# Kernel optimization log

Measured on AMD Instinct MI355X. Metric: run time of the kernel, lower is better.

The kernel has to match this reference:

```python
import jax, jax.numpy as jnp
import numpy as np

L, D, DB, P, B = 33, 2048, 1024, 24, 2048
EPS = 1e-5

def _ln(x, g, b):
    # LayerNorm over last axis, eps matches torch default 1e-5
    mu = jnp.mean(x, axis=-1, keepdims=True)
    var = jnp.mean(jnp.square(x - mu), axis=-1, keepdims=True)
    return (x - mu) * jax.lax.rsqrt(var + EPS) * g + b

def setup_inputs() -> dict:
    key = jax.random.key(0)
    ks = jax.random.split(key, 8)
    s1 = 1.0 / np.sqrt(D)   # fan-in style scaling to keep activations sane
    s2 = 1.0 / np.sqrt(DB)
    sp = 1.0 / np.sqrt(P)
    return {
        "x":      jax.random.normal(ks[0], (B, L, D), jnp.float32),
        "pos_emb": jax.random.uniform(ks[1], (L, P), jnp.float32),
        "Wk":     jax.random.normal(ks[2], (P, D), jnp.float32) * sp,
        "W1":     jax.random.normal(ks[3], (L, D, DB), jnp.float32) * s1,
        "b1":     jnp.zeros((L, DB), jnp.float32),
        "ln1_g":  jnp.ones((L, DB), jnp.float32),
        "ln1_b":  jnp.zeros((L, DB), jnp.float32),
        "W2":     jax.random.normal(ks[4], (L, DB, D), jnp.float32) * s2,
        "b2":     jnp.zeros((L, D), jnp.float32),
        "ln2_g":  jnp.ones((L, D), jnp.float32),
        "ln2_b":  jnp.zeros((L, D), jnp.float32),
        "Wq1":    jax.random.normal(ks[5], (D, DB), jnp.float32) * s1,
        "bq1":    jnp.zeros((DB,), jnp.float32),
        "lnq_g":  jnp.ones((DB,), jnp.float32),
        "lnq_b":  jnp.zeros((DB,), jnp.float32),
        "Wq2":    jax.random.normal(ks[6], (DB, D), jnp.float32) * s2,
        "bq2":    jnp.zeros((D,), jnp.float32),
    }

def reference(x, pos_emb, Wk, W1, b1, ln1_g, ln1_b, W2, b2, ln2_g, ln2_b,
              Wq1, bq1, lnq_g, lnq_b, Wq2, bq2):
    # x: [B, L, D]
    z_L = x[:, -1, :]                                   # [B, D]
    keys = pos_emb @ Wk                                 # Eq.10: [L, D]
    # Eq.11 + Eq.4: per-layer value MLPs, grouped as batched GEMMs
    h = jax.nn.gelu(jnp.einsum('bld,ldk->blk', x, W1) + b1, approximate=False)
    h = _ln(h, ln1_g, ln1_b)                            # [B, L, DB]
    v = jnp.einsum('blk,lkd->bld', h, W2) + b2          # [B, L, D]
    values = _ln(v, ln2_g, ln2_b)                       # [B, L, D]
    # Eq.5: query from last layer
    hq = jax.nn.gelu(z_L @ Wq1 + bq1, approximate=False)
    hq = _ln(hq, lnq_g, lnq_b)
    q_tr = hq @ Wq2 + bq2                               # [B, D]
    query = 1.0 + jax.nn.elu(z_L + q_tr)                # [B, D]
    # Eq.7-9: single-query attention over depth + residual
    attn = jax.nn.softmax(query @ keys.T, axis=-1)      # [B, L]
    attended = jnp.einsum('bl,bld->bd', attn, values)   # [B, D]
    return z_L + attended
```

## Files before the change

kernel.cpp:

```cpp
#include <hip/hip_runtime.h>
#include <cstddef>
#include <cstdint>

#define Lc 33
#define Dc 2048
#define DBc 1024
#define Pc 24
#define Bc 2048

typedef __attribute__((ext_vector_type(4))) float f32x4;
typedef __attribute__((ext_vector_type(8))) short s16x8;
typedef __attribute__((ext_vector_type(4))) short s16x4;

__device__ __forceinline__ short bf16r(float f) {
  unsigned u = __float_as_uint(f);
  u = (u + 0x7fffu + ((u >> 16) & 1u)) >> 16;
  return (short)u;
}
__device__ __forceinline__ float bf2f(short s) {
  return __uint_as_float(((unsigned)(unsigned short)s) << 16);
}
__device__ __forceinline__ s16x8 pack8(const float* f) {
  s16x8 r;
#pragma unroll
  for (int i = 0; i < 8; ++i) r[i] = bf16r(f[i]);
  return r;
}
__device__ __forceinline__ void split8(const float* f, s16x8& hi, s16x8& lo) {
#pragma unroll
  for (int i = 0; i < 8; ++i) {
    short h = bf16r(f[i]);
    hi[i] = h;
    lo[i] = bf16r(f[i] - bf2f(h));
  }
}
__device__ __forceinline__ void gl_lds16(const void* g, void* l) {
  __builtin_amdgcn_global_load_lds(
      (const __attribute__((address_space(1))) unsigned int*)g,
      (__attribute__((address_space(3))) unsigned int*)l, 16, 0, 0);
}

__global__ __launch_bounds__(256)
void cvt_bf16_kernel(const float* __restrict__ in,
                     unsigned short* __restrict__ outp) {
  const size_t i = ((size_t)blockIdx.x * 256 + threadIdx.x) * 8;
  f32x4 a = *(const f32x4*)(in + i);
  f32x4 b = *(const f32x4*)(in + i + 4);
  float f[8] = {a[0], a[1], a[2], a[3], b[0], b[1], b[2], b[3]};
  *(s16x8*)(outp + i) = pack8(f);
}

__global__ __launch_bounds__(256)
void keys_kernel(const float* __restrict__ pe, const float* __restrict__ Wk,
                 float* __restrict__ keys) {
  const int l = blockIdx.x;
  const int d = blockIdx.y * 256 + threadIdx.x;
  float s = 0.f;
#pragma unroll
  for (int p = 0; p < Pc; ++p) s += pe[l * Pc + p] * Wk[(size_t)p * Dc + d];
  keys[(size_t)l * Dc + d] = s;
}

template <int K, int N>
__global__ __launch_bounds__(256)
void transpose_w(const float* __restrict__ W, unsigned short* __restrict__ Wt) {
  const int z = blockIdx.z;
  const int k0 = blockIdx.x * 64, n0 = blockIdx.y * 64;
  __shared__ unsigned short tile[64][66];
  const int t = threadIdx.x;
  {
    const int r = t >> 2, cq = (t & 3) * 16;
    const float* src = W + (size_t)z * K * N + (size_t)(k0 + r) * N + n0 + cq;
#pragma unroll
    for (int i = 0; i < 16; i += 4) {
      f32x4 v = *(const f32x4*)(src + i);
#pragma unroll
      for (int j = 0; j < 4; ++j)
        tile[r][cq + i + j] = (unsigned short)bf16r(v[j]);
    }
  }
  __syncthreads();
  {
    const int n = t >> 2, kc = (t & 3) * 16;
    s16x8 o0, o1;
#pragma unroll
    for (int i = 0; i < 8; ++i) {
      o0[i] = tile[kc + i][n];
      o1[i] = tile[kc + 8 + i][n];
    }
    unsigned short* dst =
        Wt + (size_t)z * N * K + (size_t)(n0 + n) * K + k0 + kc;
    *(s16x8*)dst = o0;
    *(s16x8*)(dst + 8) = o1;
  }
}

template <int K, int N, int GELU>
__global__ __launch_bounds__(256, 2)
void gemm2ph(const unsigned short* __restrict__ A,
             const unsigned short* __restrict__ Wt,
             const float* __restrict__ bias,
             unsigned short* __restrict__ outbuf) {
  constexpr int NT = K / 64;
  const int z = blockIdx.z, bm = blockIdx.x, bn = blockIdx.y;
  const int tid = threadIdx.x, lane = tid & 63, w = tid >> 6;
  const int wr = (w >> 1) * 64, wc = (w & 1) * 64;
  const int l15 = lane & 15, kb = lane >> 4;

  __shared__ __align__(16) unsigned short Als[2][128 * 64];
  __shared__ __align__(16) unsigned short Bls[2][128 * 64];

  f32x4 acc[4][4];
#pragma unroll
  for (int m = 0; m < 4; ++m)
#pragma unroll
    for (int n = 0; n < 4; ++n) {
      acc[m][n][0] = 0.f; acc[m][n][1] = 0.f;
      acc[m][n][2] = 0.f; acc[m][n][3] = 0.f;
    }

  const int rl8 = lane >> 3, sl = lane & 7;
  const int swzE = ((sl ^ rl8) << 3);

  const unsigned short* Bbase = Wt + (size_t)z * N * K;

  auto stage = [&](int buf, int kt) {
#pragma unroll
    for (int j = 0; j < 4; ++j) {
      const int rloc = w * 32 + j * 8 + rl8;
      gl_lds16(A + ((size_t)(bm * 128 + rloc) * Lc + z) * K + kt * 64 + swzE,
               (char*)&Als[buf][0] + w * 4096 + j * 1024);
      gl_lds16(Bbase + (size_t)(bn * 128 + rloc) * K + kt * 64 + swzE,
               (char*)&Bls[buf][0] + w * 4096 + j * 1024);
    }
  };

  stage(0, 0);
  asm volatile("s_waitcnt vmcnt(0)" ::: "memory");
  __builtin_amdgcn_s_barrier();

  for (int kt = 0; kt < NT; ++kt) {
    const int cur = kt & 1;
    if (kt + 1 < NT) stage(cur ^ 1, kt + 1);
#pragma unroll
    for (int kk = 0; kk < 2; ++kk) {
      s16x8 af[4], bfv[4];
#pragma unroll
      for (int m = 0; m < 4; ++m) {
        const int row = wr + m * 16 + l15;
        const int slot = kk * 4 + kb;
        af[m] = *(const s16x8*)((const char*)&Als[cur][0] + row * 128 +
                                ((slot ^ (row & 7)) << 4));
      }
#pragma unroll
      for (int n = 0; n < 4; ++n) {
        const int row = wc + n * 16 + l15;
        const int slot = kk * 4 + kb;
        bfv[n] = *(const s16x8*)((const char*)&Bls[cur][0] + row * 128 +
                                 ((slot ^ (row & 7)) << 4));
      }
#pragma unroll
      for (int m = 0; m < 4; ++m)
#pragma unroll
        for (int n = 0; n < 4; ++n)
          acc[m][n] = __builtin_amdgcn_mfma_f32_16x16x32_bf16(
              af[m], bfv[n], acc[m][n], 0, 0, 0);
    }
    asm volatile("s_waitcnt vmcnt(0)" ::: "memory");
    __builtin_amdgcn_s_barrier();
  }

  const float* biasP = bias + (size_t)z * N;
#pragma unroll
  for (int m = 0; m < 4; ++m) {
    const int r0 = bm * 128 + wr + m * 16 + kb * 4;
#pragma unroll
    for (int n = 0; n < 4; ++n) {
      const int col = bn * 128 + wc + n * 16 + l15;
      const float bs = biasP[col];
#pragma unroll
      for (int j = 0; j < 4; ++j) {
        const int r = r0 + j;
        float v = acc[m][n][j] + bs;
        if constexpr (GELU) v = 0.5f * v * (1.0f + erff(v * 0.70710678118f));
        outbuf[((size_t)r * Lc + z) * N + col] = (unsigned short)bf16r(v);
      }
    }
  }
}

template <int MODE, int SPLITQ>
__global__ __launch_bounds__(256, 2)
void gemm_fused(const float* __restrict__ x,
                const unsigned short* __restrict__ hbuf,
                const float* __restrict__ hqF,
                const float* __restrict__ Wmain, const float* __restrict__ Wq,
                const float* __restrict__ bmain, const float* __restrict__ bq,
                unsigned short* __restrict__ outH, float* __restrict__ outHq,
                unsigned short* __restrict__ outV, float* __restrict__ outQ) {
  constexpr int K = (MODE == 1) ? 2048 : 1024;
  constexpr int N = (MODE == 1) ? 1024 : 2048;
  constexpr int BK = 32;
  constexpr int NT = K / BK;

  const int z = blockIdx.z;
  const int bm = blockIdx.x;
  const int bn = blockIdx.y;
  const int tid = threadIdx.x;
  const int lane = tid & 63;
  const int wid = tid >> 6;
  const int wr = (wid >> 1) * 64;
  const int wc = (wid & 1) * 64;
  const int l15 = lane & 15;
  const int kb = lane >> 4;

  const float* Bp = SPLITQ ? Wq : (Wmain + (size_t)z * K * N);

  __shared__ short Als[1 + SPLITQ][128][32];
  __shared__ short Bls[1 + SPLITQ][128][32];

  const f32x4 vzero = {0.f, 0.f, 0.f, 0.f};
  f32x4 acc[4][4];
#pragma unroll
  for (int m = 0; m < 4; ++m)
#pragma unroll
    for (int n = 0; n < 4; ++n) acc[m][n] = vzero;

  const int ar = tid >> 1;
  const int ak = (tid & 1) * 16;
  const int grow = bm * 128 + ar;

  const float* ApF = nullptr;
  const unsigned short* ApH = nullptr;
  if constexpr (MODE == 1) {
    const int lsel = SPLITQ ? (Lc - 1) : z;
    ApF = x + (size_t)grow * (Lc * Dc) + (size_t)lsel * Dc + ak;
  } else if constexpr (SPLITQ == 1) {
    ApF = hqF + (size_t)grow * DBc + ak;
  } else {
    ApH = hbuf + ((size_t)grow * 33 + z) * DBc + ak;
  }

  const int bnL = tid & 127;
  const int bj = tid >> 7;
  const int c0 = ((bnL >> 1) & 3) ^ bj;
  const int kc0 = c0 * 8;
  const int kc1 = (c0 ^ 2) * 8;
  const float* Bcol = Bp + (size_t)bn * 128 + bnL;

  float aF[16];
  s16x8 aH0, aH1;
  float bF[16];

  auto loadA = [&](int kt) {
    if constexpr (MODE == 2 && SPLITQ == 0) {
      const unsigned short* p = ApH + kt * BK;
      aH0 = *(const s16x8*)p;
      aH1 = *(const s16x8*)(p + 8);
    } else {
      const float* p = ApF + kt * BK;
#pragma unroll
      for (int i = 0; i < 4; ++i) {
        f32x4 t = *(const f32x4*)(p + i * 4);
#pragma unroll
        for (int j = 0; j < 4; ++j) aF[i * 4 + j] = t[j];
      }
    }
  };
  auto loadB = [&](int kt) {
    const float* p0 = Bcol + (size_t)(kt * BK + kc0) * N;
    const float* p1 = Bcol + (size_t)(kt * BK + kc1) * N;
#pragma unroll
    for (int i = 0; i < 8; ++i) bF[i] = p0[(size_t)i * N];
#pragma unroll
    for (int i = 0; i < 8; ++i) bF[8 + i] = p1[(size_t)i * N];
  };
  auto writeLDS = [&]() {
    if constexpr (MODE == 2 && SPLITQ == 0) {
      *(s16x8*)&Als[0][ar][ak] = aH0;
      *(s16x8*)&Als[0][ar][ak + 8] = aH1;
    } else if constexpr (SPLITQ == 0) {
      *(s16x8*)&Als[0][ar][ak] = pack8(aF);
      *(s16x8*)&Als[0][ar][ak + 8] = pack8(aF + 8);
    } else {
      s16x8 h0, l0, h1, l1;
      split8(aF, h0, l0);
      split8(aF + 8, h1, l1);
      *(s16x8*)&Als[0][ar][ak] = h0;
      *(s16x8*)&Als[1][ar][ak] = l0;
      *(s16x8*)&Als[0][ar][ak + 8] = h1;
      *(s16x8*)&Als[1][ar][ak + 8] = l1;
    }
    if constexpr (SPLITQ == 0) {
      *(s16x8*)&Bls[0][bnL][kc0] = pack8(bF);
      *(s16x8*)&Bls[0][bnL][kc1] = pack8(bF + 8);
    } else {
      s16x8 h0, l0, h1, l1;
      split8(bF, h0, l0);
      split8(bF + 8, h1, l1);
      *(s16x8*)&Bls[0][bnL][kc0] = h0;
      *(s16x8*)&Bls[1][bnL][kc0] = l0;
      *(s16x8*)&Bls[0][bnL][kc1] = h1;
      *(s16x8*)&Bls[1][bnL][kc1] = l1;
    }
  };

  loadA(0);
  loadB(0);
  for (int kt = 0; kt < NT; ++kt) {
    __syncthreads();
    writeLDS();
    if (kt + 1 < NT) {
      loadA(kt + 1);
      loadB(kt + 1);
    }
    __syncthreads();
    s16x8 af[4], bfv[4];
#pragma unroll
    for (int m = 0; m < 4; ++m)
      af[m] = *(const s16x8*)&Als[0][wr + m * 16 + l15][kb * 8];
#pragma unroll
    for (int n = 0; n < 4; ++n)
      bfv[n] = *(const s16x8*)&Bls[0][wc + n * 16 + l15][kb * 8];
    if constexpr (SPLITQ == 1) {
      s16x8 afl[4], bfl[4];
#pragma unroll
      for (int m = 0; m < 4; ++m)
        afl[m] = *(const s16x8*)&Als[1][wr + m * 16 + l15][kb * 8];
#pragma unroll
      for (int n = 0; n < 4; ++n)
        bfl[n] = *(const s16x8*)&Bls[1][wc + n * 16 + l15][kb * 8];
#pragma unroll
      for (int m = 0; m < 4; ++m)
#pragma unroll
        for (int n = 0; n < 4; ++n) {
          acc[m][n] = __builtin_amdgcn_mfma_f32_16x16x32_bf16(
              af[m], bfv[n], acc[m][n], 0, 0, 0);
          acc[m][n] = __builtin_amdgcn_mfma_f32_16x16x32_bf16(
              af[m], bfl[n], acc[m][n], 0, 0, 0);
          acc[m][n] = __builtin_amdgcn_mfma_f32_16x16x32_bf16(
              afl[m], bfv[n], acc[m][n], 0, 0, 0);
        }
    } else {
#pragma unroll
      for (int m = 0; m < 4; ++m)
#pragma unroll
        for (int n = 0; n < 4; ++n)
          acc[m][n] = __builtin_amdgcn_mfma_f32_16x16x32_bf16(
              af[m], bfv[n], acc[m][n], 0, 0, 0);
    }
  }

  const float* biasP = SPLITQ ? bq : (bmain + (size_t)z * N);
#pragma unroll
  for (int m = 0; m < 4; ++m) {
    const int r0 = bm * 128 + wr + m * 16 + kb * 4;
#pragma unroll
    for (int n = 0; n < 4; ++n) {
      const int col = bn * 128 + wc + n * 16 + l15;
      const float bs = biasP[col];
#pragma unroll
      for (int j = 0; j < 4; ++j) {
        const int r = r0 + j;
        const float v = acc[m][n][j] + bs;
        if constexpr (MODE == 1 && SPLITQ == 0) {
          const float g = 0.5f * v * (1.0f + erff(v * 0.70710678118f));
          outH[((size_t)r * 33 + z) * DBc + col] = (unsigned short)bf16r(g);
        } else if constexpr (MODE == 1 && SPLITQ == 1) {
          const float g = 0.5f * v * (1.0f + erff(v * 0.70710678118f));
          outHq[(size_t)r * DBc + col] = g;
        } else if constexpr (MODE == 2 && SPLITQ == 0) {
          outV[((size_t)r * 33 + z) * Dc + col] = (unsigned short)bf16r(v);
        } else {
          const float zl =
              x[(size_t)r * (Lc * Dc) + (size_t)(Lc - 1) * Dc + col];
          const float t = zl + v;
          outQ[(size_t)r * Dc + col] = (t > 0.f) ? (1.f + t) : __expf(t);
        }
      }
    }
  }
}

template <int W>
__global__ __launch_bounds__(256)
void ln_kernel(unsigned short* __restrict__ buf, const float* __restrict__ gmain,
               const float* __restrict__ bmain) {
  constexpr int E = W / 256;
  const int z = blockIdx.x;
  const int b = blockIdx.y;
  const int tid = threadIdx.x;
  unsigned short* row = buf + ((size_t)b * 33 + z) * W;
  float v[E];
  if constexpr (E == 4) {
    s16x4 t = *(const s16x4*)(row + tid * 4);
#pragma unroll
    for (int i = 0; i < 4; ++i) v[i] = bf2f(t[i]);
  } else {
    s16x8 t = *(const s16x8*)(row + tid * 8);
#pragma unroll
    for (int i = 0; i < 8; ++i) v[i] = bf2f(t[i]);
  }
  float s = 0.f, s2 = 0.f;
#pragma unroll
  for (int i = 0; i < E; ++i) {
    s += v[i];
    s2 += v[i] * v[i];
  }
#pragma unroll
  for (int o = 32; o > 0; o >>= 1) {
    s += __shfl_xor(s, o);
    s2 += __shfl_xor(s2, o);
  }
  __shared__ float red[2][4];
  const int w = tid >> 6;
  if ((tid & 63) == 0) {
    red[0][w] = s;
    red[1][w] = s2;
  }
  __syncthreads();
  s = red[0][0] + red[0][1] + red[0][2] + red[0][3];
  s2 = red[1][0] + red[1][1] + red[1][2] + red[1][3];
  const float mu = s * (1.0f / W);
  const float var = s2 * (1.0f / W) - mu * mu;
  const float rstd = rsqrtf(var + 1e-5f);
  const float* G = gmain + (size_t)z * W;
  const float* Bt = bmain + (size_t)z * W;
  if constexpr (E == 4) {
    f32x4 gv = *(const f32x4*)(G + tid * 4);
    f32x4 bv = *(const f32x4*)(Bt + tid * 4);
    s16x4 o;
#pragma unroll
    for (int i = 0; i < 4; ++i)
      o[i] = bf16r((v[i] - mu) * rstd * gv[i] + bv[i]);
    *(s16x4*)(row + tid * 4) = o;
  } else {
    f32x4 g0 = *(const f32x4*)(G + tid * 8);
    f32x4 g1 = *(const f32x4*)(G + tid * 8 + 4);
    f32x4 b0 = *(const f32x4*)(Bt + tid * 8);
    f32x4 b1 = *(const f32x4*)(Bt + tid * 8 + 4);
    s16x8 o;
#pragma unroll
    for (int i = 0; i < 4; ++i) {
      o[i] = bf16r((v[i] - mu) * rstd * g0[i] + b0[i]);
      o[i + 4] = bf16r((v[i + 4] - mu) * rstd * g1[i] + b1[i]);
    }
    *(s16x8*)(row + tid * 8) = o;
  }
}

__global__ __launch_bounds__(256)
void ln_f32_kernel(float* __restrict__ buf, const float* __restrict__ g,
                   const float* __restrict__ bb) {
  const int r = blockIdx.x;
  const int tid = threadIdx.x;
  float* row = buf + (size_t)r * DBc;
  f32x4 v = *(const f32x4*)(row + tid * 4);
  float s = 0.f, s2 = 0.f;
#pragma unroll
  for (int i = 0; i < 4; ++i) {
    s += v[i];
    s2 += v[i] * v[i];
  }
#pragma unroll
  for (int o = 32; o > 0; o >>= 1) {
    s += __shfl_xor(s, o);
    s2 += __shfl_xor(s2, o);
  }
  __shared__ float red[2][4];
  const int w = tid >> 6;
  if ((tid & 63) == 0) {
    red[0][w] = s;
    red[1][w] = s2;
  }
  __syncthreads();
  s = red[0][0] + red[0][1] + red[0][2] + red[0][3];
  s2 = red[1][0] + red[1][1] + red[1][2] + red[1][3];
  const float mu = s * (1.0f / DBc);
  const float var = s2 * (1.0f / DBc) - mu * mu;
  const float rstd = rsqrtf(var + 1e-5f);
  f32x4 gv = *(const f32x4*)(g + tid * 4);
  f32x4 bv = *(const f32x4*)(bb + tid * 4);
  f32x4 o;
#pragma unroll
  for (int i = 0; i < 4; ++i) o[i] = (v[i] - mu) * rstd * gv[i] + bv[i];
  *(f32x4*)(row + tid * 4) = o;
}

__global__ __launch_bounds__(256)
void attn_kernel(const float* __restrict__ x, const float* __restrict__ query,
                 const float* __restrict__ keys,
                 const unsigned short* __restrict__ vals,
                 float* __restrict__ out) {
  const int b = blockIdx.x;
  const int tid = threadIdx.x;
  const int d0 = tid * 8;

  float q[8];
  {
    f32x4 t0 = *(const f32x4*)(query + (size_t)b * Dc + d0);
    f32x4 t1 = *(const f32x4*)(query + (size_t)b * Dc + d0 + 4);
#pragma unroll
    for (int i = 0; i < 4; ++i) {
      q[i] = t0[i];
      q[i + 4] = t1[i];
    }
  }
  float s[33];
#pragma unroll
  for (int l = 0; l < 33; ++l) {
    const float* kp = keys + (size_t)l * Dc + d0;
    f32x4 k0 = *(const f32x4*)kp;
    f32x4 k1 = *(const f32x4*)(kp + 4);
    float t = 0.f;
#pragma unroll
    for (int i = 0; i < 4; ++i) t += q[i] * k0[i] + q[i + 4] * k1[i];
    s[l] = t;
  }
#pragma unroll
  for (int l = 0; l < 33; ++l) {
    float v = s[l];
#pragma unroll
    for (int o = 32; o > 0; o >>= 1) v += __shfl_xor(v, o);
    s[l] = v;
  }
  __shared__ float sred[4][33];
  __shared__ float sl[33];
  const int w = tid >> 6;
  if ((tid & 63) == 0) {
#pragma unroll
    for (int l = 0; l < 33; ++l) sred[w][l] = s[l];
  }
  __syncthreads();
  if (tid < 33)
    sl[tid] = sred[0][tid] + sred[1][tid] + sred[2][tid] + sred[3][tid];
  __syncthreads();

  float m = -1e30f;
#pragma unroll
  for (int l = 0; l < 33; ++l) m = fmaxf(m, sl[l]);
  float p[33];
  float sum = 0.f;
#pragma unroll
  for (int l = 0; l < 33; ++l) {
    p[l] = __expf(sl[l] - m);
    sum += p[l];
  }
  const float inv = 1.0f / sum;

  float acc8[8];
  {
    const float* zl = x + (size_t)b * (Lc * Dc) + (size_t)(Lc - 1) * Dc + d0;
    f32x4 z0 = *(const f32x4*)zl;
    f32x4 z1 = *(const f32x4*)(zl + 4);
#pragma unroll
    for (int i = 0; i < 4; ++i) {
      acc8[i] = z0[i];
      acc8[i + 4] = z1[i];
    }
  }
  const unsigned short* vb = vals + (size_t)b * 33 * Dc + d0;
#pragma unroll
  for (int l = 0; l < 33; ++l) {
    s16x8 vv = *(const s16x8*)(vb + (size_t)l * Dc);
    const float a = p[l] * inv;
#pragma unroll
    for (int i = 0; i < 8; ++i) acc8[i] += a * bf2f(vv[i]);
  }
  f32x4 o0, o1;
#pragma unroll
  for (int i = 0; i < 4; ++i) {
    o0[i] = acc8[i];
    o1[i] = acc8[i + 4];
  }
  *(f32x4*)(out + (size_t)b * Dc + d0) = o0;
  *(f32x4*)(out + (size_t)b * Dc + d0 + 4) = o1;
}

extern "C" void kernel_launch(void* const* d_in, const int* in_sizes, int n_in,
                              void* d_out, int out_size, void* d_ws,
                              size_t ws_size, hipStream_t stream) {
  const float* x = (const float*)d_in[0];
  const float* pe = (const float*)d_in[1];
  const float* Wk = (const float*)d_in[2];
  const float* W1 = (const float*)d_in[3];
  const float* b1 = (const float*)d_in[4];
  const float* ln1g = (const float*)d_in[5];
  const float* ln1b = (const float*)d_in[6];
  const float* W2 = (const float*)d_in[7];
  const float* b2 = (const float*)d_in[8];
  const float* ln2g = (const float*)d_in[9];
  const float* ln2b = (const float*)d_in[10];
  const float* Wq1 = (const float*)d_in[11];
  const float* bq1 = (const float*)d_in[12];
  const float* lnqg = (const float*)d_in[13];
  const float* lnqb = (const float*)d_in[14];
  const float* Wq2 = (const float*)d_in[15];
  const float* bq2 = (const float*)d_in[16];
  float* out = (float*)d_out;
  char* ws = (char*)d_ws;

  float* keysP = (float*)(ws);
  float* queryP = (float*)(ws + 270336);
  float* hqP = (float*)(ws + 17047552);
  unsigned short* hP = (unsigned short*)(ws + 25436160);
  unsigned short* xbfP = (unsigned short*)(ws + 163848192);
  unsigned short* valsP = (unsigned short*)(ws + 163848192);
  unsigned short* W1tP = (unsigned short*)(ws + 440672256);
  unsigned short* W2tP = (unsigned short*)(ws + 440672256);

  const bool fast = (ws_size >= 579084288ull);

  keys_kernel<<<dim3(33, 8), 256, 0, stream>>>(pe, Wk, keysP);

  gemm_fused<1, 1><<<dim3(16, 8, 1), 256, 0, stream>>>(
      x, nullptr, nullptr, nullptr, Wq1, nullptr, bq1, nullptr, hqP, nullptr,
      nullptr);

  if (fast) {
    cvt_bf16_kernel<<<dim3(67584), 256, 0, stream>>>(x, xbfP);
    transpose_w<2048, 1024><<<dim3(32, 16, 33), 256, 0, stream>>>(W1, W1tP);
    gemm2ph<2048, 1024, 1><<<dim3(16, 8, 33), 256, 0, stream>>>(xbfP, W1tP,
                                                                b1, hP);
  } else {
    gemm_fused<1, 0><<<dim3(16, 8, 33), 256, 0, stream>>>(
        x, nullptr, nullptr, W1, nullptr, b1, nullptr, hP, nullptr, nullptr,
        nullptr);
  }

  ln_kernel<1024><<<dim3(33, 2048), 256, 0, stream>>>(hP, ln1g, ln1b);

  ln_f32_kernel<<<dim3(2048), 256, 0, stream>>>(hqP, lnqg, lnqb);

  if (fast) {
    transpose_w<1024, 2048><<<dim3(16, 32, 33), 256, 0, stream>>>(W2, W2tP);
    gemm2ph<1024, 2048, 0><<<dim3(16, 16, 33), 256, 0, stream>>>(hP, W2tP, b2,
                                                                 valsP);
  } else {
    gemm_fused<2, 0><<<dim3(16, 16, 33), 256, 0, stream>>>(
        x, hP, nullptr, W2, nullptr, b2, nullptr, nullptr, nullptr, valsP,
        nullptr);
  }

  gemm_fused<2, 1><<<dim3(16, 16, 1), 256, 0, stream>>>(
      x, nullptr, hqP, nullptr, Wq2, nullptr, bq2, nullptr, nullptr, nullptr,
      queryP);

  ln_kernel<2048><<<dim3(33, 2048), 256, 0, stream>>>(valsP, ln2g, ln2b);

  attn_kernel<<<dim3(2048), 256, 0, stream>>>(x, queryP, keysP, valsP, out);
}
```

Before: 1.722 ms.

## Use 256x256 GEMM tiles with XCD remap and fuse LN2 stats into epilogue

Replaces the 128x128 two-phase GEMM with a 512-thread 256x256 tile kernel using BK=32 and an XCD-aware workgroup remap. The W2 GEMM epilogue accumulates per-row sum and sum-of-squares into a stats buffer via atomics. The attention kernel then applies LayerNorm on the fly, removing the separate ln_kernel pass over the values tensor. The aim is better operand reuse and one fewer full read-write of a large tensor. In exchange it adds atomics, a memset, larger register pressure, and LN computed from bf16-rounded values using a one-pass variance.

```diff
diff --git a/kernel.cpp b/kernel.cpp
--- a/kernel.cpp
+++ b/kernel.cpp
@@ -95,43 +95,53 @@
   }
 }
 
-template <int K, int N, int GELU>
-__global__ __launch_bounds__(256, 2)
-void gemm2ph(const unsigned short* __restrict__ A,
+template <int K, int N, int NBM, int NBN, int GELU, int STATS>
+__global__ __launch_bounds__(512, 2)
+void gemm256(const unsigned short* __restrict__ A,
              const unsigned short* __restrict__ Wt,
              const float* __restrict__ bias,
-             unsigned short* __restrict__ outbuf) {
-  constexpr int NT = K / 64;
-  const int z = blockIdx.z, bm = blockIdx.x, bn = blockIdx.y;
-  const int tid = threadIdx.x, lane = tid & 63, w = tid >> 6;
-  const int wr = (w >> 1) * 64, wc = (w & 1) * 64;
-  const int l15 = lane & 15, kb = lane >> 4;
-
-  __shared__ __align__(16) unsigned short Als[2][128 * 64];
-  __shared__ __align__(16) unsigned short Bls[2][128 * 64];
-
-  f32x4 acc[4][4];
-#pragma unroll
-  for (int m = 0; m < 4; ++m)
+             unsigned short* __restrict__ outbuf, float* __restrict__ stats) {
+  constexpr int NT = K / 32;
+  constexpr int nwg = 33 * NBM * NBN;
+  constexpr int q = nwg >> 3, r = nwg & 7;
+  const int orig = blockIdx.x;
+  const int xcd = orig & 7;
+  const int wgid =
+      ((xcd < r) ? xcd * (q + 1) : r * (q + 1) + (xcd - r) * q) + (orig >> 3);
+  const int z = wgid / (NBM * NBN);
+  const int rem = wgid - z * (NBM * NBN);
+  const int bm = rem / NBN;
+  const int bn = rem - bm * NBN;
+
+  const int tid = threadIdx.x, lane = tid & 63, wv = tid >> 6;
+  const int wm = wv >> 2, wn = wv & 3;
+  const int wr = wm * 128, wc = wn * 64;
+  const int l15 = lane & 15, l4 = lane >> 4;
+
+  __shared__ __align__(16) unsigned short Als[2][256 * 32];
+  __shared__ __align__(16) unsigned short Bls[2][256 * 32];
+
+  f32x4 acc[8][4];
+#pragma unroll
+  for (int m = 0; m < 8; ++m)
 #pragma unroll
     for (int n = 0; n < 4; ++n) {
       acc[m][n][0] = 0.f; acc[m][n][1] = 0.f;
       acc[m][n][2] = 0.f; acc[m][n][3] = 0.f;
     }
 
-  const int rl8 = lane >> 3, sl = lane & 7;
-  const int swzE = ((sl ^ rl8) << 3);
-
+  const int rA = lane >> 2, sA = lane & 3;
   const unsigned short* Bbase = Wt + (size_t)z * N * K;
 
   auto stage = [&](int buf, int kt) {
 #pragma unroll
-    for (int j = 0; j < 4; ++j) {
-      const int rloc = w * 32 + j * 8 + rl8;
-      gl_lds16(A + ((size_t)(bm * 128 + rloc) * Lc + z) * K + kt * 64 + swzE,
-               (char*)&Als[buf][0] + w * 4096 + j * 1024);
-      gl_lds16(Bbase + (size_t)(bn * 128 + rloc) * K + kt * 64 + swzE,
-               (char*)&Bls[buf][0] + w * 4096 + j * 1024);
+    for (int c = 0; c < 2; ++c) {
+      const int rl = wv * 32 + c * 16 + rA;
+      const int swz = (sA ^ (rl & 3)) * 8;
+      gl_lds16(A + ((size_t)(bm * 256 + rl) * Lc + z) * K + kt * 32 + swz,
+               (char*)&Als[buf][0] + wv * 2048 + c * 1024);
+      gl_lds16(Bbase + (size_t)(bn * 256 + rl) * K + kt * 32 + swz,
+               (char*)&Bls[buf][0] + wv * 2048 + c * 1024);
     }
   };
 
@@ -142,48 +152,59 @@
   for (int kt = 0; kt < NT; ++kt) {
     const int cur = kt & 1;
     if (kt + 1 < NT) stage(cur ^ 1, kt + 1);
-#pragma unroll
-    for (int kk = 0; kk < 2; ++kk) {
-      s16x8 af[4], bfv[4];
-#pragma unroll
-      for (int m = 0; m < 4; ++m) {
-        const int row = wr + m * 16 + l15;
-        const int slot = kk * 4 + kb;
-        af[m] = *(const s16x8*)((const char*)&Als[cur][0] + row * 128 +
-                                ((slot ^ (row & 7)) << 4));
-      }
-#pragma unroll
-      for (int n = 0; n < 4; ++n) {
-        const int row = wc + n * 16 + l15;
-        const int slot = kk * 4 + kb;
-        bfv[n] = *(const s16x8*)((const char*)&Bls[cur][0] + row * 128 +
-                                 ((slot ^ (row & 7)) << 4));
-      }
-#pragma unroll
-      for (int m = 0; m < 4; ++m)
-#pragma unroll
-        for (int n = 0; n < 4; ++n)
-          acc[m][n] = __builtin_amdgcn_mfma_f32_16x16x32_bf16(
-              af[m], bfv[n], acc[m][n], 0, 0, 0);
+    s16x8 bfv[4];
+#pragma unroll
+    for (int n = 0; n < 4; ++n) {
+      const int row = wc + n * 16 + l15;
+      bfv[n] = *(const s16x8*)((const char*)&Bls[cur][0] + row * 64 +
+                               ((l4 ^ (row & 3)) << 4));
+    }
+#pragma unroll
+    for (int m = 0; m < 8; ++m) {
+      const int row = wr + m * 16 + l15;
+      s16x8 af = *(const s16x8*)((const char*)&Als[cur][0] + row * 64 +
+                                 ((l4 ^ (row & 3)) << 4));
+#pragma unroll
+      for (int n = 0; n < 4; ++n)
+        acc[m][n] = __builtin_amdgcn_mfma_f32_16x16x32_bf16(af, bfv[n],
+                                                            acc[m][n], 0, 0, 0);
     }
     asm volatile("s_waitcnt vmcnt(0)" ::: "memory");
     __builtin_amdgcn_s_barrier();
   }
 
   const float* biasP = bias + (size_t)z * N;
-#pragma unroll
-  for (int m = 0; m < 4; ++m) {
-    const int r0 = bm * 128 + wr + m * 16 + kb * 4;
-#pragma unroll
-    for (int n = 0; n < 4; ++n) {
-      const int col = bn * 128 + wc + n * 16 + l15;
-      const float bs = biasP[col];
-#pragma unroll
-      for (int j = 0; j < 4; ++j) {
-        const int r = r0 + j;
-        float v = acc[m][n][j] + bs;
+  float bsv[4];
+#pragma unroll
+  for (int n = 0; n < 4; ++n) bsv[n] = biasP[bn * 256 + wc + n * 16 + l15];
+
+#pragma unroll
+  for (int m = 0; m < 8; ++m) {
+#pragma unroll
+    for (int j = 0; j < 4; ++j) {
+      const int grow = bm * 256 + wr + m * 16 + l4 * 4 + j;
+      float s1 = 0.f, s2 = 0.f;
+#pragma unroll
+      for (int n = 0; n < 4; ++n) {
+        const int col = bn * 256 + wc + n * 16 + l15;
+        float v = acc[m][n][j] + bsv[n];
         if constexpr (GELU) v = 0.5f * v * (1.0f + erff(v * 0.70710678118f));
-        outbuf[((size_t)r * Lc + z) * N + col] = (unsigned short)bf16r(v);
+        outbuf[((size_t)grow * Lc + z) * N + col] = (unsigned short)bf16r(v);
+        if constexpr (STATS) {
+          s1 += v;
+          s2 += v * v;
+        }
+      }
+      if constexpr (STATS) {
+#pragma unroll
+        for (int o = 1; o < 16; o <<= 1) {
+          s1 += __shfl_xor(s1, o);
+          s2 += __shfl_xor(s2, o);
+        }
+        if (l15 == 0) {
+          atomicAdd(&stats[((size_t)grow * Lc + z) * 2 + 0], s1);
+          atomicAdd(&stats[((size_t)grow * Lc + z) * 2 + 1], s2);
+        }
       }
     }
   }
@@ -450,6 +471,41 @@
 }
 
 __global__ __launch_bounds__(256)
+void stats_kernel(const unsigned short* __restrict__ vals,
+                  float* __restrict__ stats) {
+  const int z = blockIdx.x;
+  const int b = blockIdx.y;
+  const int tid = threadIdx.x;
+  const unsigned short* row = vals + ((size_t)b * 33 + z) * Dc;
+  s16x8 t = *(const s16x8*)(row + tid * 8);
+  float s = 0.f, s2 = 0.f;
+#pragma unroll
+  for (int i = 0; i < 8; ++i) {
+    float v = bf2f(t[i]);
+    s += v;
+    s2 += v * v;
+  }
+#pragma unroll
+  for (int o = 32; o > 0; o >>= 1) {
+    s += __shfl_xor(s, o);
+    s2 += __shfl_xor(s2, o);
+  }
+  __shared__ float red[2][4];
+  const int w = tid >> 6;
+  if ((tid & 63) == 0) {
+    red[0][w] = s;
+    red[1][w] = s2;
+  }
+  __syncthreads();
+  if (tid == 0) {
+    stats[((size_t)b * 33 + z) * 2 + 0] =
+        red[0][0] + red[0][1] + red[0][2] + red[0][3];
+    stats[((size_t)b * 33 + z) * 2 + 1] =
+        red[1][0] + red[1][1] + red[1][2] + red[1][3];
+  }
+}
+
+__global__ __launch_bounds__(256)
 void ln_f32_kernel(float* __restrict__ buf, const float* __restrict__ g,
                    const float* __restrict__ bb) {
   const int r = blockIdx.x;
@@ -491,19 +547,20 @@
 void attn_kernel(const float* __restrict__ x, const float* __restrict__ query,
                  const float* __restrict__ keys,
                  const unsigned short* __restrict__ vals,
-                 float* __restrict__ out) {
+                 const float* __restrict__ stats, const float* __restrict__ g2,
+                 const float* __restrict__ b2ln, float* __restrict__ out) {
   const int b = blockIdx.x;
   const int tid = threadIdx.x;
   const int d0 = tid * 8;
 
-  float q[8];
+  float qv[8];
   {
     f32x4 t0 = *(const f32x4*)(query + (size_t)b * Dc + d0);
     f32x4 t1 = *(const f32x4*)(query + (size_t)b * Dc + d0 + 4);
 #pragma unroll
     for (int i = 0; i < 4; ++i) {
-      q[i] = t0[i];
-      q[i + 4] = t1[i];
+      qv[i] = t0[i];
+      qv[i + 4] = t1[i];
     }
   }
   float s[33];
@@ -514,7 +571,7 @@
     f32x4 k1 = *(const f32x4*)(kp + 4);
     float t = 0.f;
 #pragma unroll
-    for (int i = 0; i < 4; ++i) t += q[i] * k0[i] + q[i + 4] * k1[i];
+    for (int i = 0; i < 4; ++i) t += qv[i] * k0[i] + qv[i + 4] * k1[i];
     s[l] = t;
   }
 #pragma unroll
@@ -562,10 +619,22 @@
   const unsigned short* vb = vals + (size_t)b * 33 * Dc + d0;
 #pragma unroll
   for (int l = 0; l < 33; ++l) {
+    const float st0 = stats[((size_t)b * 33 + l) * 2 + 0];
+    const float st1 = stats[((size_t)b * 33 + l) * 2 + 1];
+    const float mu = st0 * (1.0f / Dc);
+    const float var = st1 * (1.0f / Dc) - mu * mu;
+    const float rstd = rsqrtf(var + 1e-5f);
+    const float a = p[l] * inv;
     s16x8 vv = *(const s16x8*)(vb + (size_t)l * Dc);
-    const float a = p[l] * inv;
-#pragma unroll
-    for (int i = 0; i < 8; ++i) acc8[i] += a * bf2f(vv[i]);
+    const float* gp = g2 + (size_t)l * Dc + d0;
+    const float* bp = b2ln + (size_t)l * Dc + d0;
+    f32x4 g0 = *(const f32x4*)gp, g1 = *(const f32x4*)(gp + 4);
+    f32x4 b0 = *(const f32x4*)bp, b1 = *(const f32x4*)(bp + 4);
+#pragma unroll
+    for (int i = 0; i < 4; ++i) {
+      acc8[i] += a * ((bf2f(vv[i]) - mu) * rstd * g0[i] + b0[i]);
+      acc8[i + 4] += a * ((bf2f(vv[i + 4]) - mu) * rstd * g1[i] + b1[i]);
+    }
   }
   f32x4 o0, o1;
 #pragma unroll
@@ -603,13 +672,14 @@
   float* keysP = (float*)(ws);
   float* queryP = (float*)(ws + 270336);
   float* hqP = (float*)(ws + 17047552);
-  unsigned short* hP = (unsigned short*)(ws + 25436160);
-  unsigned short* xbfP = (unsigned short*)(ws + 163848192);
-  unsigned short* valsP = (unsigned short*)(ws + 163848192);
-  unsigned short* W1tP = (unsigned short*)(ws + 440672256);
-  unsigned short* W2tP = (unsigned short*)(ws + 440672256);
-
-  const bool fast = (ws_size >= 579084288ull);
+  float* statsP = (float*)(ws + 25436160);
+  unsigned short* hP = (unsigned short*)(ws + 25976832);
+  unsigned short* xbfP = (unsigned short*)(ws + 164388864);
+  unsigned short* valsP = (unsigned short*)(ws + 164388864);
+  unsigned short* W1tP = (unsigned short*)(ws + 441212928);
+  unsigned short* W2tP = (unsigned short*)(ws + 441212928);
+
+  const bool fast = (ws_size >= 579624960ull);
 
   keys_kernel<<<dim3(33, 8), 256, 0, stream>>>(pe, Wk, keysP);
 
@@ -620,8 +690,8 @@
   if (fast) {
     cvt_bf16_kernel<<<dim3(67584), 256, 0, stream>>>(x, xbfP);
     transpose_w<2048, 1024><<<dim3(32, 16, 33), 256, 0, stream>>>(W1, W1tP);
-    gemm2ph<2048, 1024, 1><<<dim3(16, 8, 33), 256, 0, stream>>>(xbfP, W1tP,
-                                                                b1, hP);
+    gemm256<2048, 1024, 8, 4, 1, 0><<<dim3(33 * 8 * 4), 512, 0, stream>>>(
+        xbfP, W1tP, b1, hP, nullptr);
   } else {
     gemm_fused<1, 0><<<dim3(16, 8, 33), 256, 0, stream>>>(
         x, nullptr, nullptr, W1, nullptr, b1, nullptr, hP, nullptr, nullptr,
@@ -632,21 +702,23 @@
 
   ln_f32_kernel<<<dim3(2048), 256, 0, stream>>>(hqP, lnqg, lnqb);
 
+  hipMemsetAsync(statsP, 0, 2048 * 33 * 2 * sizeof(float), stream);
+
   if (fast) {
     transpose_w<1024, 2048><<<dim3(16, 32, 33), 256, 0, stream>>>(W2, W2tP);
-    gemm2ph<1024, 2048, 0><<<dim3(16, 16, 33), 256, 0, stream>>>(hP, W2tP, b2,
-                                                                 valsP);
+    gemm256<1024, 2048, 8, 8, 0, 1><<<dim3(33 * 8 * 8), 512, 0, stream>>>(
+        hP, W2tP, b2, valsP, statsP);
   } else {
     gemm_fused<2, 0><<<dim3(16, 16, 33), 256, 0, stream>>>(
         x, hP, nullptr, W2, nullptr, b2, nullptr, nullptr, nullptr, valsP,
         nullptr);
+    stats_kernel<<<dim3(33, 2048), 256, 0, stream>>>(valsP, statsP);
   }
 
   gemm_fused<2, 1><<<dim3(16, 16, 1), 256, 0, stream>>>(
       x, nullptr, hqP, nullptr, Wq2, nullptr, bq2, nullptr, nullptr, nullptr,
       queryP);
 
-  ln_kernel<2048><<<dim3(33, 2048), 256, 0, stream>>>(valsP, ln2g, ln2b);
-
-  attn_kernel<<<dim3(2048), 256, 0, stream>>>(x, queryP, keysP, valsP, out);
-}
+  attn_kernel<<<dim3(2048), 256, 0, stream>>>(x, queryP, keysP, valsP, statsP,
+                                              ln2g, ln2b, out);
+}
```

Result: slower. 1.910 ms (+10.9%).
